# Kernel tuning notes

Hardware: AMD Instinct MI355X
Metric: run time of the kernel (lower is better)

## Reference

```python
import jax, jax.numpy as jnp
import numpy as np

HEADS = 8
DIM_HEAD = 64


def setup_inputs() -> dict:
    key = jax.random.key(0)
    ks = jax.random.split(key, 4)
    B, C, H, W = 1, 256, 64, 64
    inner = HEADS * DIM_HEAD  # 512
    x = jax.random.normal(ks[0], (B, C, H, W), dtype=jnp.float32)
    norm_w = jnp.ones((C,), dtype=jnp.float32)                      # RMSNorm weight (1,C,1,1) flattened
    w_qkv = jax.random.normal(ks[1], (3 * inner, C), dtype=jnp.float32) * 0.02  # 1x1 conv, no bias
    w_out = jax.random.normal(ks[2], (C, inner), dtype=jnp.float32) * 0.02      # 1x1 conv
    b_out = jax.random.normal(ks[3], (C,), dtype=jnp.float32) * 0.02
    return {"x": x, "norm_w": norm_w, "w_qkv": w_qkv, "w_out": w_out, "b_out": b_out}


def reference(x, norm_w, w_qkv, w_out, b_out):
    B, C, H, W = x.shape
    N = H * W
    # RMSNorm: F.normalize over channel dim (L2, eps clamp) * weight * sqrt(C)
    l2 = jnp.sqrt(jnp.sum(x * x, axis=1, keepdims=True))
    xn = x / jnp.maximum(l2, 1e-12) * norm_w[None, :, None, None] * (C ** 0.5)
    # 1x1 conv QKV = channel matmul
    qkv = jnp.einsum('oc,bchw->bohw', w_qkv, xn)  # [B, 3*inner, H, W]
    q, k, v = jnp.split(qkv, 3, axis=1)

    def split_heads(t):
        # 'b (h d) x y -> b h (x y) d'
        return t.reshape(B, HEADS, DIM_HEAD, N).transpose(0, 1, 3, 2)

    q, k, v = map(split_heads, (q, k, v))
    scale = DIM_HEAD ** -0.5
    scores = jnp.einsum('bhnd,bhmd->bhnm', q, k) * scale  # [B,H,N,N]
    attn = jax.nn.softmax(scores, axis=-1)
    out = jnp.einsum('bhnm,bhmd->bhnd', attn, v)
    # 'b h (x y) d -> b (h d) x y'
    out = out.transpose(0, 1, 3, 2).reshape(B, HEADS * DIM_HEAD, H, W)
    # output 1x1 conv + residual (note: residual is the NORMALIZED x, per source)
    return jnp.einsum('ci,bihw->bchw', w_out, out) + b_out[None, :, None, None] + xn
```

## Files before the change

kernel.cpp:

```cpp
#include <hip/hip_runtime.h>


#define NPIX 4096
#define CIN 256
#define INNER 512
#define NHEAD 8
#define DH 64

typedef _Float16 f16;
typedef __attribute__((ext_vector_type(8))) _Float16 f16x8;
typedef __attribute__((ext_vector_type(4))) float f32x4;

static __device__ __forceinline__ f32x4 mfma_f16(f16x8 a, f16x8 b, f32x4 c) {
  return __builtin_amdgcn_mfma_f32_16x16x32_f16(a, b, c, 0, 0, 0);
}

static __device__ __forceinline__ unsigned pk2(float lo, float hi) {
  return __builtin_bit_cast(unsigned, __builtin_amdgcn_cvt_pkrtz(lo, hi));
}

__global__ __launch_bounds__(256) void k_cvt(const float* __restrict__ a,
                                             f16* __restrict__ b, int n) {
  int i = blockIdx.x * 256 + threadIdx.x;
  if (i < n) b[i] = (f16)a[i];
}

__global__ __launch_bounds__(256) void k_rmsnorm(const float* __restrict__ x,
                                                 const float* __restrict__ w,
                                                 float* __restrict__ xn,
                                                 f16* __restrict__ xnT) {
  const int pi = threadIdx.x & 15, cs = threadIdx.x >> 4;
  const int p = blockIdx.x * 16 + pi;
  __shared__ float red[16][16];
  float xv[16];
  float ss = 0.f;
#pragma unroll
  for (int i = 0; i < 16; ++i) {
    xv[i] = x[(cs * 16 + i) * NPIX + p];
    ss += xv[i] * xv[i];
  }
  red[cs][pi] = ss;
  __syncthreads();
  float tot = 0.f;
#pragma unroll
  for (int s = 0; s < 16; ++s) tot += red[s][pi];
  float inv = 16.0f / fmaxf(sqrtf(tot), 1e-12f);
  union { f16x8 v[2]; f16 h[16]; } hv;
#pragma unroll
  for (int i = 0; i < 16; ++i) {
    int c = cs * 16 + i;
    float v = xv[i] * inv * w[c];
    xn[c * NPIX + p] = v;
    hv.h[i] = (f16)v;
  }
  *(f16x8*)(xnT + (size_t)p * CIN + cs * 16) = hv.v[0];
  *(f16x8*)(xnT + (size_t)p * CIN + cs * 16 + 8) = hv.v[1];
}

__global__ __launch_bounds__(256) void k_qkv(const f16* __restrict__ wqkv,
                                             const f16* __restrict__ xnT,
                                             f16* __restrict__ qT,
                                             f16* __restrict__ kT,
                                             f16* __restrict__ vv) {
  const int lane = threadIdx.x & 63, wave = threadIdx.x >> 6;
  const int l15 = lane & 15, quad = lane >> 4;
  const int obase = blockIdx.y * 64 + (wave >> 1) * 32;
  const int pbase = blockIdx.x * 128 + (wave & 1) * 64;
  const int sect = blockIdx.y >> 3;
  f32x4 acc[8];
#pragma unroll
  for (int i = 0; i < 8; ++i) acc[i] = (f32x4){0.f, 0.f, 0.f, 0.f};
#pragma unroll
  for (int kc = 0; kc < CIN / 32; ++kc) {
    f16x8 af[2], bfr[4];
#pragma unroll
    for (int oc = 0; oc < 2; ++oc)
      af[oc] = *(const f16x8*)(wqkv + (size_t)(obase + oc * 16 + l15) * CIN + kc * 32 + quad * 8);
#pragma unroll
    for (int pc = 0; pc < 4; ++pc)
      bfr[pc] = *(const f16x8*)(xnT + (size_t)(pbase + pc * 16 + l15) * CIN + kc * 32 + quad * 8);
    if (sect < 2) {
#pragma unroll
      for (int pc = 0; pc < 4; ++pc)
#pragma unroll
        for (int oc = 0; oc < 2; ++oc)
          acc[pc * 2 + oc] = mfma_f16(bfr[pc], af[oc], acc[pc * 2 + oc]);
    } else {
#pragma unroll
      for (int oc = 0; oc < 2; ++oc)
#pragma unroll
        for (int pc = 0; pc < 4; ++pc)
          acc[oc * 4 + pc] = mfma_f16(af[oc], bfr[pc], acc[oc * 4 + pc]);
    }
  }
  if (sect < 2) {
    f16* dst = (sect == 0) ? qT : kT;
    const float sc = (sect == 0) ? 0.18033688f : 1.0f;
    const int head = blockIdx.y & 7;
    const int dd = (wave >> 1) * 32;
#pragma unroll
    for (int pc = 0; pc < 4; ++pc)
#pragma unroll
      for (int oc = 0; oc < 2; ++oc)
#pragma unroll
        for (int r = 0; r < 4; ++r) {
          int p = pbase + pc * 16 + quad * 4 + r;
          dst[((size_t)(head << 12) + p) * DH + dd + oc * 16 + l15] =
              (f16)(acc[pc * 2 + oc][r] * sc);
        }
  } else {
#pragma unroll
    for (int oc = 0; oc < 2; ++oc)
#pragma unroll
      for (int r = 0; r < 4; ++r) {
        int o = obase + oc * 16 + quad * 4 + r - 2 * INNER;
#pragma unroll
        for (int pc = 0; pc < 4; ++pc)
          vv[(size_t)o * NPIX + pbase + pc * 16 + l15] = (f16)acc[oc * 4 + pc][r];
      }
  }
}

__global__ __launch_bounds__(512) void k_attn(const f16* __restrict__ qT,
                                              const f16* __restrict__ kT,
                                              const f16* __restrict__ vv,
                                              f16* __restrict__ Ows) {
  const int head = blockIdx.x & 7;
  const int qb = (blockIdx.x >> 3) * 128;
  const int tid = threadIdx.x;
  const int wave = tid >> 6, lane = tid & 63;
  const int l15 = lane & 15, quad = lane >> 4;

  extern __shared__ float smem[];
  float (*Om)[4][64][17] = reinterpret_cast<float (*)[4][64][17]>(smem);
  float (*Ll)[4][16]     = reinterpret_cast<float (*)[4][16]>(smem + 8 * 4 * 64 * 17);

  f16x8 qf[8][2];
#pragma unroll
  for (int qt = 0; qt < 8; ++qt)
#pragma unroll
    for (int kc = 0; kc < 2; ++kc)
      qf[qt][kc] = *(const f16x8*)(qT + ((size_t)(head << 12) + qb + qt * 16 + l15) * DH + kc * 32 + quad * 8);

  f32x4 o[8][4];
  float ol[8];
#pragma unroll
  for (int qt = 0; qt < 8; ++qt) {
#pragma unroll
    for (int c = 0; c < 4; ++c) o[qt][c] = (f32x4){0.f, 0.f, 0.f, 0.f};
    ol[qt] = 0.f;
  }

  const f16* kbase = kT + (size_t)(head << 12) * DH;
  const f16* vbase = vv + (size_t)(head * DH) * NPIX;
  const int kb0 = wave * (NPIX / 8);
  const int srcA = ((quad & 1) << 5) + l15;
  const int srcB = srcA + 16;
  const bool hiQuad = quad >= 2;

  for (int it = 0; it < 16; ++it) {
    const int kb = kb0 + it * 32;
    f16x8 kf[2][2];
#pragma unroll
    for (int nc = 0; nc < 2; ++nc)
#pragma unroll
      for (int kc = 0; kc < 2; ++kc)
        kf[nc][kc] = *(const f16x8*)(kbase + (size_t)(kb + nc * 16 + l15) * DH + kc * 32 + quad * 8);
    f16x8 vf[4];
#pragma unroll
    for (int c = 0; c < 4; ++c)
      vf[c] = *(const f16x8*)(vbase + (size_t)(c * 16 + l15) * NPIX + kb + quad * 8);

#pragma unroll
    for (int qt = 0; qt < 8; ++qt) {
      f32x4 s0 = mfma_f16(kf[0][0], qf[qt][0], (f32x4){0.f, 0.f, 0.f, 0.f});
      s0 = mfma_f16(kf[0][1], qf[qt][1], s0);
      f32x4 s1 = mfma_f16(kf[1][0], qf[qt][0], (f32x4){0.f, 0.f, 0.f, 0.f});
      s1 = mfma_f16(kf[1][1], qf[qt][1], s1);
      float p0[4], p1[4];
#pragma unroll
      for (int r = 0; r < 4; ++r) {
        p0[r] = __builtin_amdgcn_exp2f(s0[r]);
        p1[r] = __builtin_amdgcn_exp2f(s1[r]);
      }
      float ps = ((p0[0] + p0[1]) + (p0[2] + p0[3])) +
                 ((p1[0] + p1[1]) + (p1[2] + p1[3]));
      ps += __shfl_xor(ps, 16);
      ps += __shfl_xor(ps, 32);
      ol[qt] += ps;
      unsigned A0 = pk2(p0[0], p0[1]), B0 = pk2(p0[2], p0[3]);
      unsigned A1 = pk2(p1[0], p1[1]), B1 = pk2(p1[2], p1[3]);
      unsigned As = hiQuad ? A1 : A0;
      unsigned Bs = hiQuad ? B1 : B0;
      union { f16x8 v; unsigned u[4]; } pf;
      pf.u[0] = (unsigned)__shfl((int)As, srcA);
      pf.u[1] = (unsigned)__shfl((int)Bs, srcA);
      pf.u[2] = (unsigned)__shfl((int)As, srcB);
      pf.u[3] = (unsigned)__shfl((int)Bs, srcB);
#pragma unroll
      for (int c = 0; c < 4; ++c) o[qt][c] = mfma_f16(vf[c], pf.v, o[qt][c]);
    }
  }

#pragma unroll
  for (int pass = 0; pass < 2; ++pass) {
    if (pass) __syncthreads();
#pragma unroll
    for (int qt2 = 0; qt2 < 4; ++qt2) {
      const int qt = pass * 4 + qt2;
      if (quad == 0) Ll[wave][qt2][l15] = ol[qt];
#pragma unroll
      for (int c = 0; c < 4; ++c)
#pragma unroll
        for (int r = 0; r < 4; ++r)
          Om[wave][qt2][c * 16 + quad * 4 + r][l15] = o[qt][c][r];
    }
    __syncthreads();
    const int d = tid & 63;
    const int mqt = wave >> 1, qh = (wave & 1) * 8;
#pragma unroll
    for (int j = 0; j < 8; ++j) {
      const int q = qh + j;
      float O = 0.f, L = 0.f;
#pragma unroll
      for (int w = 0; w < 8; ++w) {
        O += Om[w][mqt][d][q];
        L += Ll[w][mqt][q];
      }
      Ows[((size_t)(head << 12) + qb + (pass * 4 + mqt) * 16 + q) * DH + d] =
          (f16)(O / L);
    }
  }
}

__global__ __launch_bounds__(256) void k_oproj(const f16* __restrict__ wout,
                                               const f16* __restrict__ Ows,
                                               const float* __restrict__ bout,
                                               const float* __restrict__ xn,
                                               float* __restrict__ out) {
  const int lane = threadIdx.x & 63, wave = threadIdx.x >> 6;
  const int l15 = lane & 15, quad = lane >> 4;
  const int mbase = blockIdx.y * 32 + (wave >> 1) * 16;
  const int pbase = blockIdx.x * 64 + (wave & 1) * 32;
  f32x4 acc[2];
  acc[0] = (f32x4){0.f, 0.f, 0.f, 0.f};
  acc[1] = (f32x4){0.f, 0.f, 0.f, 0.f};
#pragma unroll
  for (int kc = 0; kc < INNER / 32; ++kc) {
    f16x8 af = *(const f16x8*)(wout + (size_t)(mbase + l15) * INNER + kc * 32 + quad * 8);
    int i0 = kc * 32 + quad * 8;
    int head = i0 >> 6, d0 = i0 & 63;
#pragma unroll
    for (int pc = 0; pc < 2; ++pc) {
      f16x8 bfr = *(const f16x8*)(Ows + ((size_t)(head << 12) + pbase + pc * 16 + l15) * DH + d0);
      acc[pc] = mfma_f16(af, bfr, acc[pc]);
    }
  }
#pragma unroll
  for (int pc = 0; pc < 2; ++pc)
#pragma unroll
    for (int r = 0; r < 4; ++r) {
      int c = mbase + quad * 4 + r, p = pbase + pc * 16 + l15;
      out[c * NPIX + p] = acc[pc][r] + bout[c] + xn[c * NPIX + p];
    }
}

extern "C" void kernel_launch(void* const* d_in, const int* in_sizes, int n_in,
                              void* d_out, int out_size, void* d_ws, size_t ws_size,
                              hipStream_t stream) {
  (void)in_sizes; (void)n_in; (void)out_size; (void)ws_size;
  const float* x      = (const float*)d_in[0];
  const float* norm_w = (const float*)d_in[1];
  const float* w_qkv  = (const float*)d_in[2];
  const float* w_out  = (const float*)d_in[3];
  const float* b_out  = (const float*)d_in[4];
  float* out = (float*)d_out;

  char* ws = (char*)d_ws;
  float* xn    = (float*)(ws);
  f16* xnT     = (f16*)(ws + (4u << 20));
  f16* qT      = (f16*)(ws + (6u << 20));
  f16* kT      = (f16*)(ws + (10u << 20));
  f16* vv      = (f16*)(ws + (14u << 20));
  f16* Ows     = (f16*)(ws + (18u << 20));
  f16* wqkv_h  = (f16*)(ws + (22u << 20));
  f16* wout_h  = (f16*)(ws + (23u << 20));

  hipLaunchKernelGGL(k_cvt, dim3((3 * INNER * CIN + 255) / 256), dim3(256), 0, stream,
                     w_qkv, wqkv_h, 3 * INNER * CIN);
  hipLaunchKernelGGL(k_cvt, dim3((CIN * INNER + 255) / 256), dim3(256), 0, stream,
                     w_out, wout_h, CIN * INNER);
  hipLaunchKernelGGL(k_rmsnorm, dim3(NPIX / 16), dim3(256), 0, stream, x, norm_w, xn, xnT);
  hipLaunchKernelGGL(k_qkv, dim3(NPIX / 128, 1536 / 64), dim3(256), 0, stream,
                     wqkv_h, xnT, qT, kT, vv);
  hipLaunchKernelGGL(k_attn, dim3(256), dim3(512), 141312, stream,
                     qT, kT, vv, Ows);
  hipLaunchKernelGGL(k_oproj, dim3(NPIX / 64, CIN / 32), dim3(256), 0, stream,
                     wout_h, Ows, b_out, xn, out);
}
```

Baseline: 172.2 us.

## Software-pipeline attention score MFMAs, defer row-sum shuffles, merge weight conversions

The attention inner loop now computes the next query tile's QK^T scores while the current tile's exp and PV MFMAs run, and raises wave priority around the MFMA groups with s_setprio. The per-iteration cross-lane reductions of the softmax denominator are moved out of the loop so they run once at the end. __shfl calls are replaced with direct ds_bpermute, and launch bounds now request two blocks per CU. The two weight-conversion launches are merged into one kernel writing a contiguous buffer. The pipelining raises register pressure, and the occupancy hint may force spills.

```diff
diff --git a/kernel.cpp b/kernel.cpp
--- a/kernel.cpp
+++ b/kernel.cpp
@@ -19,10 +19,12 @@
   return __builtin_bit_cast(unsigned, __builtin_amdgcn_cvt_pkrtz(lo, hi));
 }
 
-__global__ __launch_bounds__(256) void k_cvt(const float* __restrict__ a,
-                                             f16* __restrict__ b, int n) {
+__global__ __launch_bounds__(256) void k_cvt2(const float* __restrict__ a1, int n1,
+                                              const float* __restrict__ a2, int n2,
+                                              f16* __restrict__ b) {
   int i = blockIdx.x * 256 + threadIdx.x;
-  if (i < n) b[i] = (f16)a[i];
+  if (i < n1) b[i] = (f16)a1[i];
+  else if (i < n1 + n2) b[i] = (f16)a2[i - n1];
 }
 
 __global__ __launch_bounds__(256) void k_rmsnorm(const float* __restrict__ x,
@@ -121,10 +123,10 @@
   }
 }
 
-__global__ __launch_bounds__(512) void k_attn(const f16* __restrict__ qT,
-                                              const f16* __restrict__ kT,
-                                              const f16* __restrict__ vv,
-                                              f16* __restrict__ Ows) {
+__global__ __launch_bounds__(512, 2) void k_attn(const f16* __restrict__ qT,
+                                                 const f16* __restrict__ kT,
+                                                 const f16* __restrict__ vv,
+                                                 f16* __restrict__ Ows) {
   const int head = blockIdx.x & 7;
   const int qb = (blockIdx.x >> 3) * 128;
   const int tid = threadIdx.x;
@@ -154,8 +156,8 @@
   const f16* kbase = kT + (size_t)(head << 12) * DH;
   const f16* vbase = vv + (size_t)(head * DH) * NPIX;
   const int kb0 = wave * (NPIX / 8);
-  const int srcA = ((quad & 1) << 5) + l15;
-  const int srcB = srcA + 16;
+  const int srcA4 = (((quad & 1) << 5) + l15) * 4;
+  const int srcB4 = srcA4 + 64;
   const bool hiQuad = quad >= 2;
 
   for (int it = 0; it < 16; ++it) {
@@ -171,35 +173,55 @@
     for (int c = 0; c < 4; ++c)
       vf[c] = *(const f16x8*)(vbase + (size_t)(c * 16 + l15) * NPIX + kb + quad * 8);
 
+#define S_QT(QT, S)                                                       \
+  do {                                                                    \
+    S[0] = mfma_f16(kf[0][0], qf[QT][0], (f32x4){0.f, 0.f, 0.f, 0.f});    \
+    S[0] = mfma_f16(kf[0][1], qf[QT][1], S[0]);                           \
+    S[1] = mfma_f16(kf[1][0], qf[QT][0], (f32x4){0.f, 0.f, 0.f, 0.f});    \
+    S[1] = mfma_f16(kf[1][1], qf[QT][1], S[1]);                           \
+  } while (0)
+
+    f32x4 sc[2], sn[2];
+    __builtin_amdgcn_s_setprio(1);
+    S_QT(0, sc);
+    __builtin_amdgcn_s_setprio(0);
 #pragma unroll
     for (int qt = 0; qt < 8; ++qt) {
-      f32x4 s0 = mfma_f16(kf[0][0], qf[qt][0], (f32x4){0.f, 0.f, 0.f, 0.f});
-      s0 = mfma_f16(kf[0][1], qf[qt][1], s0);
-      f32x4 s1 = mfma_f16(kf[1][0], qf[qt][0], (f32x4){0.f, 0.f, 0.f, 0.f});
-      s1 = mfma_f16(kf[1][1], qf[qt][1], s1);
+      if (qt < 7) {
+        __builtin_amdgcn_s_setprio(1);
+        S_QT(qt + 1, sn);
+        __builtin_amdgcn_s_setprio(0);
+      }
       float p0[4], p1[4];
 #pragma unroll
       for (int r = 0; r < 4; ++r) {
-        p0[r] = __builtin_amdgcn_exp2f(s0[r]);
-        p1[r] = __builtin_amdgcn_exp2f(s1[r]);
+        p0[r] = __builtin_amdgcn_exp2f(sc[0][r]);
+        p1[r] = __builtin_amdgcn_exp2f(sc[1][r]);
       }
-      float ps = ((p0[0] + p0[1]) + (p0[2] + p0[3])) +
-                 ((p1[0] + p1[1]) + (p1[2] + p1[3]));
-      ps += __shfl_xor(ps, 16);
-      ps += __shfl_xor(ps, 32);
-      ol[qt] += ps;
+      ol[qt] += ((p0[0] + p0[1]) + (p0[2] + p0[3])) +
+                ((p1[0] + p1[1]) + (p1[2] + p1[3]));
       unsigned A0 = pk2(p0[0], p0[1]), B0 = pk2(p0[2], p0[3]);
       unsigned A1 = pk2(p1[0], p1[1]), B1 = pk2(p1[2], p1[3]);
       unsigned As = hiQuad ? A1 : A0;
       unsigned Bs = hiQuad ? B1 : B0;
       union { f16x8 v; unsigned u[4]; } pf;
-      pf.u[0] = (unsigned)__shfl((int)As, srcA);
-      pf.u[1] = (unsigned)__shfl((int)Bs, srcA);
-      pf.u[2] = (unsigned)__shfl((int)As, srcB);
-      pf.u[3] = (unsigned)__shfl((int)Bs, srcB);
+      pf.u[0] = (unsigned)__builtin_amdgcn_ds_bpermute(srcA4, (int)As);
+      pf.u[1] = (unsigned)__builtin_amdgcn_ds_bpermute(srcA4, (int)Bs);
+      pf.u[2] = (unsigned)__builtin_amdgcn_ds_bpermute(srcB4, (int)As);
+      pf.u[3] = (unsigned)__builtin_amdgcn_ds_bpermute(srcB4, (int)Bs);
+      __builtin_amdgcn_s_setprio(1);
 #pragma unroll
       for (int c = 0; c < 4; ++c) o[qt][c] = mfma_f16(vf[c], pf.v, o[qt][c]);
-    }
+      __builtin_amdgcn_s_setprio(0);
+      if (qt < 7) { sc[0] = sn[0]; sc[1] = sn[1]; }
+    }
+#undef S_QT
+  }
+
+#pragma unroll
+  for (int qt = 0; qt < 8; ++qt) {
+    ol[qt] += __shfl_xor(ol[qt], 16);
+    ol[qt] += __shfl_xor(ol[qt], 32);
   }
 
 #pragma unroll
@@ -284,12 +306,11 @@
   f16* vv      = (f16*)(ws + (14u << 20));
   f16* Ows     = (f16*)(ws + (18u << 20));
   f16* wqkv_h  = (f16*)(ws + (22u << 20));
-  f16* wout_h  = (f16*)(ws + (23u << 20));
-
-  hipLaunchKernelGGL(k_cvt, dim3((3 * INNER * CIN + 255) / 256), dim3(256), 0, stream,
-                     w_qkv, wqkv_h, 3 * INNER * CIN);
-  hipLaunchKernelGGL(k_cvt, dim3((CIN * INNER + 255) / 256), dim3(256), 0, stream,
-                     w_out, wout_h, CIN * INNER);
+  f16* wout_h  = (f16*)(ws + (22u << 20) + 786432);
+
+  const int n1 = 3 * INNER * CIN, n2 = CIN * INNER;
+  hipLaunchKernelGGL(k_cvt2, dim3((n1 + n2 + 255) / 256), dim3(256), 0, stream,
+                     w_qkv, n1, w_out, n2, wqkv_h);
   hipLaunchKernelGGL(k_rmsnorm, dim3(NPIX / 16), dim3(256), 0, stream, x, norm_w, xn, xnT);
   hipLaunchKernelGGL(k_qkv, dim3(NPIX / 128, 1536 / 64), dim3(256), 0, stream,
                      wqkv_h, xnT, qT, kT, vv);
```

After: 169.1 us. About the same (-1.8%).
